# Kernel optimization log

Measured on AMD Instinct MI355X. Metric: run time of the kernel, lower is better.

Reference implementation:

```python
import jax, jax.numpy as jnp
import numpy as np

N_NODES = 50000
N_EDGES = 600000
DIM_H = 128
LN_EPS = 1e-5


def setup_inputs() -> dict:
    key = jax.random.key(0)
    ks = jax.random.split(key, 8)
    s = 1.0 / np.sqrt(DIM_H)
    return {
        "nodes": jax.random.normal(ks[0], (N_NODES, DIM_H), jnp.float32),
        "W_msg": jax.random.normal(ks[1], (DIM_H, DIM_H), jnp.float32) * s,
        "b_msg": jnp.zeros((DIM_H,), jnp.float32),
        "w_ih": jax.random.normal(ks[2], (3 * DIM_H, DIM_H), jnp.float32) * s,
        "w_hh": jax.random.normal(ks[3], (3 * DIM_H, DIM_H), jnp.float32) * s,
        "b_ih": jnp.zeros((3 * DIM_H,), jnp.float32),
        "b_hh": jnp.zeros((3 * DIM_H,), jnp.float32),
        "ln_gamma": jnp.ones((DIM_H,), jnp.float32),
        "ln_beta": jnp.zeros((DIM_H,), jnp.float32),
        "edge_src": jax.random.randint(ks[4], (N_EDGES,), 0, N_NODES, jnp.int32),
        "edge_dst": jax.random.randint(ks[5], (N_EDGES,), 0, N_NODES, jnp.int32),
    }


def _layer_norm(x, gamma, beta):
    mu = jnp.mean(x, axis=-1, keepdims=True)
    var = jnp.mean(jnp.square(x - mu), axis=-1, keepdims=True)
    return gamma * (x - mu) * jax.lax.rsqrt(var + LN_EPS) + beta


def reference(nodes, W_msg, b_msg, w_ih, w_hh, b_ih, b_hh, ln_gamma, ln_beta,
              edge_src, edge_dst):
    n_nodes = nodes.shape[0]
    # send_and_recv: per-edge message from source node, sum-reduce at dest
    msg_e = nodes[edge_src] @ W_msg.T + b_msg            # [E, H] (irregular gather)
    messages = jax.ops.segment_sum(msg_e, edge_dst, num_segments=n_nodes)  # [N, H]
    # global connection: add mean node feature
    msg = messages + jnp.mean(nodes, axis=0)
    # single-step GRU (torch gate layout: r, z, n)
    gi = msg @ w_ih.T + b_ih                             # [N, 3H]
    gh = nodes @ w_hh.T + b_hh                           # [N, 3H]
    i_r, i_z, i_n = jnp.split(gi, 3, axis=-1)
    h_r, h_z, h_n = jnp.split(gh, 3, axis=-1)
    r = jax.nn.sigmoid(i_r + h_r)
    z = jax.nn.sigmoid(i_z + h_z)
    n = jnp.tanh(i_n + r * h_n)
    h_next = (1.0 - z) * n + z * nodes
    # LayerNorm then post-GRU spatial residual with messages
    out = _layer_norm(h_next, ln_gamma, ln_beta)
    out = out + messages
    return out
```

## Files before the change

kernel.cpp:

```cpp
#include <hip/hip_runtime.h>
#include <hip/hip_bf16.h>

#define N_NODES 50000
#define N_EDGES 600000
#define DIM_H   128
#define NPAD    50048
#define NB_SCAN 196

typedef __attribute__((ext_vector_type(8))) short bf16x8;
typedef __attribute__((ext_vector_type(4))) float f32x4;
typedef __attribute__((ext_vector_type(4))) short short4v;

__device__ __forceinline__ short f2bs(float f) {
    __hip_bfloat16 h = __float2bfloat16(f);
    return *reinterpret_cast<short*>(&h);
}
__device__ __forceinline__ float bs2f(short s) {
    unsigned u = ((unsigned)(unsigned short)s) << 16;
    return __builtin_bit_cast(float, u);
}
__device__ __forceinline__ float sigm(float x) { return 1.f / (1.f + __expf(-x)); }
__device__ __forceinline__ float tanh_f(float x) {
    return 2.f / (1.f + __expf(-2.f * x)) - 1.f;
}
__device__ __forceinline__ unsigned pk2(float a, float b) {
    return ((unsigned)(unsigned short)f2bs(b) << 16) | (unsigned)(unsigned short)f2bs(a);
}
__device__ __forceinline__ float unlo(unsigned u) { return bs2f((short)(u & 0xffffu)); }
__device__ __forceinline__ float unhi(unsigned u) { return bs2f((short)(u >> 16)); }

__device__ __forceinline__ void dma16(const void* g, const void* lds_uniform) {
    __builtin_amdgcn_global_load_lds(
        (const __attribute__((address_space(1))) void*)g,
        (__attribute__((address_space(3))) void*)(unsigned)(unsigned long long)lds_uniform,
        16, 0, 0);
}

__global__ __launch_bounds__(256) void prep_k(int* __restrict__ cnt,
                                              float* __restrict__ colsum,
                                              short* __restrict__ aggTail,
                                              short* __restrict__ nodesTail) {
    int i = blockIdx.x * 256 + threadIdx.x;
    if (i < N_NODES) cnt[i] = 0;
    if (i < 128) colsum[i] = 0.f;
    if (i < 1536) {
        short4v z = {0, 0, 0, 0};
        *(short4v*)(aggTail   + i * 4) = z;
        *(short4v*)(nodesTail + i * 4) = z;
    }
}

__global__ __launch_bounds__(256) void ch_k(const float* __restrict__ nodes,
                                            float* __restrict__ colsum,
                                            short* __restrict__ nodesB,
                                            const int* __restrict__ edst,
                                            int* __restrict__ cnt) {
    const int tid = threadIdx.x;
    {
        int e = (blockIdx.x * 256 + tid) * 4;
        if (e + 3 < N_EDGES) {
            int4 d = *(const int4*)(edst + e);
            atomicAdd(&cnt[d.x], 1); atomicAdd(&cnt[d.y], 1);
            atomicAdd(&cnt[d.z], 1); atomicAdd(&cnt[d.w], 1);
        } else {
            for (; e < N_EDGES; ++e) atomicAdd(&cnt[edst[e]], 1);
        }
    }
    __shared__ float red[8][128];
    const int cg = tid & 31;
    const int rl = tid >> 5;
    float4 acc = {0.f, 0.f, 0.f, 0.f};
    for (int r = blockIdx.x * 8 + rl; r < N_NODES; r += gridDim.x * 8) {
        float4 v = *(const float4*)(nodes + (size_t)r * DIM_H + cg * 4);
        acc.x += v.x; acc.y += v.y; acc.z += v.z; acc.w += v.w;
        *(short4v*)(nodesB + (size_t)r * DIM_H + cg * 4) =
            (short4v){f2bs(v.x), f2bs(v.y), f2bs(v.z), f2bs(v.w)};
    }
    *(float4*)&red[rl][cg * 4] = acc;
    __syncthreads();
    if (tid < 128) {
        float s = 0.f;
#pragma unroll
        for (int i = 0; i < 8; ++i) s += red[i][tid];
        unsafeAtomicAdd(&colsum[tid], s);
    }
}

__global__ __launch_bounds__(256) void scan_k(const int* __restrict__ cnt,
                                              int* __restrict__ rowptr,
                                              int* __restrict__ pos,
                                              const float* __restrict__ wmsg,
                                              const float* __restrict__ wih,
                                              const float* __restrict__ whh,
                                              short* __restrict__ wmsgB,
                                              short* __restrict__ wihB,
                                              short* __restrict__ whhB) {
    const int b = blockIdx.x, t = threadIdx.x;
    const int lane = t & 63, w = t >> 6;
    __shared__ int red[4];
    __shared__ int wsum[4];

    {
        const int gid = b * 256 + t;
        const int gsz = NB_SCAN * 256;
        for (int i = gid; i < 49152; i += gsz) {
            wihB[i] = f2bs(wih[i]);
            whhB[i] = f2bs(whh[i]);
        }
        if (gid < 16384) wmsgB[gid] = f2bs(wmsg[gid]);
    }

    int tot = 0;
    const int lim = b * 256;
    for (int i = t * 4; i < lim; i += 1024) {
        int4 v = *(const int4*)(cnt + i);
        tot += (v.x + v.y) + (v.z + v.w);
    }
#pragma unroll
    for (int o = 32; o; o >>= 1) tot += __shfl_xor(tot, o, 64);
    if (lane == 0) red[w] = tot;
    __syncthreads();
    const int offset = red[0] + red[1] + red[2] + red[3];

    int i = b * 256 + t;
    int v = (i < N_NODES) ? cnt[i] : 0;
    int x = v;
#pragma unroll
    for (int o = 1; o < 64; o <<= 1) {
        int y = __shfl_up(x, o, 64);
        if (lane >= o) x += y;
    }
    if (lane == 63) wsum[w] = x;
    __syncthreads();
    int woff = 0;
#pragma unroll
    for (int j = 0; j < 4; ++j)
        if (j < w) woff += wsum[j];
    int excl = offset + woff + (x - v);
    if (i < N_NODES) { rowptr[i] = excl; pos[i] = excl; }
    if (i == N_NODES - 1) rowptr[N_NODES] = excl + v;
}

__global__ __launch_bounds__(256) void reorder_k(const int* __restrict__ esrc,
                                                 const int* __restrict__ edst,
                                                 int* __restrict__ pos,
                                                 int* __restrict__ ssrc) {
    int e = (blockIdx.x * 256 + threadIdx.x) * 4;
    if (e + 3 < N_EDGES) {
        int4 s = *(const int4*)(esrc + e);
        int4 d = *(const int4*)(edst + e);
        ssrc[atomicAdd(&pos[d.x], 1)] = s.x;
        ssrc[atomicAdd(&pos[d.y], 1)] = s.y;
        ssrc[atomicAdd(&pos[d.z], 1)] = s.z;
        ssrc[atomicAdd(&pos[d.w], 1)] = s.w;
    } else {
        for (; e < N_EDGES; ++e) {
            int p = atomicAdd(&pos[edst[e]], 1);
            ssrc[p] = esrc[e];
        }
    }
}

__global__ __launch_bounds__(256) void aggregate_k(const short* __restrict__ nodesB,
                                                   const int* __restrict__ rowptr,
                                                   const int* __restrict__ ssrc,
                                                   short* __restrict__ aggB) {
    const int wid = threadIdx.x >> 6;
    const int lane = threadIdx.x & 63;
    const int g = lane >> 4, l = lane & 15;
    const int n = blockIdx.x * 4 + wid;
    if (n >= N_NODES) return;
    const int s0 = rowptr[n], s1 = rowptr[n + 1];

    float accf[8] = {0.f, 0.f, 0.f, 0.f, 0.f, 0.f, 0.f, 0.f};
    int e = s0 + g;
    for (; e + 4 < s1; e += 8) {
        int sa = ssrc[e], sb = ssrc[e + 4];
        bf16x8 va = *(const bf16x8*)(nodesB + (size_t)sa * DIM_H + l * 8);
        bf16x8 vb = *(const bf16x8*)(nodesB + (size_t)sb * DIM_H + l * 8);
#pragma unroll
        for (int k = 0; k < 8; ++k) accf[k] += bs2f(va[k]) + bs2f(vb[k]);
    }
    if (e < s1) {
        int sa = ssrc[e];
        bf16x8 va = *(const bf16x8*)(nodesB + (size_t)sa * DIM_H + l * 8);
#pragma unroll
        for (int k = 0; k < 8; ++k) accf[k] += bs2f(va[k]);
    }
#pragma unroll
    for (int k = 0; k < 8; ++k) {
        accf[k] += __shfl_xor(accf[k], 32, 64);
        accf[k] += __shfl_xor(accf[k], 16, 64);
    }
    if (g == 0) {
        uint4 ov;
        ov.x = pk2(accf[0], accf[1]);
        ov.y = pk2(accf[2], accf[3]);
        ov.z = pk2(accf[4], accf[5]);
        ov.w = pk2(accf[6], accf[7]);
        *(uint4*)(aggB + (size_t)n * DIM_H + l * 8) = ov;
    }
}

__global__ __launch_bounds__(512) void fused_k(const short* __restrict__ aggB,
                                               const short* __restrict__ nodesB,
                                               const short* __restrict__ wmsgB,
                                               const short* __restrict__ wihB,
                                               const short* __restrict__ whhB,
                                               const float* __restrict__ bmsg,
                                               const float* __restrict__ bih,
                                               const float* __restrict__ bhh,
                                               const int* __restrict__ deg,
                                               const float* __restrict__ colsum,
                                               const float* __restrict__ gamma,
                                               const float* __restrict__ beta,
                                               float* __restrict__ out) {
    __shared__ short Ms[128 * 128];
    __shared__ short Wb[2][64 * 128];
    __shared__ float biasL[1280];

    const int tid = threadIdx.x;
    const int lane = tid & 63, w = tid >> 6;
    const int m0 = blockIdx.x * 128;
    const int r16 = lane & 15, qh = lane >> 4;
    const int wm = w * 16;
    const float invN = 1.0f / N_NODES;

    if (tid < 384) {
        biasL[tid]       = bih[tid];
        biasL[384 + tid] = bhh[tid];
    }
    if (tid < 128) {
        biasL[768  + tid] = bmsg[tid];
        biasL[896  + tid] = colsum[tid] * invN;
        biasL[1024 + tid] = gamma[tid];
        biasL[1152 + tid] = beta[tid];
    }

    bf16x8 aggF[4], nodF[4], msgF[4];
    const size_t rowA = (size_t)(m0 + wm + r16) * 128;
#pragma unroll
    for (int kt = 0; kt < 4; ++kt) {
        aggF[kt] = *(const bf16x8*)(aggB   + rowA + ((kt << 2) + qh) * 8);
        nodF[kt] = *(const bf16x8*)(nodesB + rowA + ((kt << 2) + qh) * 8);
    }
    int4 dgi = *(const int4*)(deg + m0 + wm + qh * 4);

#define STAGE_W(SRC, ROW0, BUF) do {                                         \
    _Pragma("unroll") for (int it = 0; it < 2; ++it) {                       \
        int c = w * 2 + it;                                                  \
        int s = c * 64 + lane;                                               \
        int r = s >> 4, q = s & 15;                                          \
        int g = q ^ (r & 15);                                                \
        dma16((SRC) + (((size_t)((ROW0) + r)) << 7) + (g << 3),              \
              &Wb[BUF][0] + (size_t)c * 512);                                \
    } } while (0)

    STAGE_W(wmsgB, 0, 0);

    f32x4 acc[2][4];
    unsigned rp[2][4][2], inp[2][4][2], np_[2][4][2];

#define CHUNK(BUF, AF, H, RST) do {                                          \
    __builtin_amdgcn_s_setprio(1);                                           \
    _Pragma("unroll") for (int kt = 0; kt < 4; ++kt) {                       \
        const int sq = (((kt << 2) + qh) ^ r16) << 3;                        \
        bf16x8 b0 = *(const bf16x8*)&Wb[BUF][(r16     ) * 128 + sq];         \
        bf16x8 b1 = *(const bf16x8*)&Wb[BUF][(r16 + 16) * 128 + sq];         \
        bf16x8 b2 = *(const bf16x8*)&Wb[BUF][(r16 + 32) * 128 + sq];         \
        bf16x8 b3 = *(const bf16x8*)&Wb[BUF][(r16 + 48) * 128 + sq];         \
        f32x4 z4 = {0.f, 0.f, 0.f, 0.f};                                     \
        acc[H][0] = __builtin_amdgcn_mfma_f32_16x16x32_bf16(                 \
            AF[kt], b0, ((RST) && kt == 0) ? z4 : acc[H][0], 0, 0, 0);       \
        acc[H][1] = __builtin_amdgcn_mfma_f32_16x16x32_bf16(                 \
            AF[kt], b1, ((RST) && kt == 0) ? z4 : acc[H][1], 0, 0, 0);       \
        acc[H][2] = __builtin_amdgcn_mfma_f32_16x16x32_bf16(                 \
            AF[kt], b2, ((RST) && kt == 0) ? z4 : acc[H][2], 0, 0, 0);       \
        acc[H][3] = __builtin_amdgcn_mfma_f32_16x16x32_bf16(                 \
            AF[kt], b3, ((RST) && kt == 0) ? z4 : acc[H][3], 0, 0, 0);       \
    }                                                                        \
    __builtin_amdgcn_s_setprio(0);                                           \
    } while (0)

    __syncthreads(); STAGE_W(wmsgB,  64, 1); CHUNK(0, aggF, 0, 1);
    __syncthreads(); STAGE_W(wihB,    0, 0); CHUNK(1, aggF, 1, 1);

    {
        float dgf[4];
        dgf[0] = (m0 + wm + qh * 4 + 0 < N_NODES) ? (float)dgi.x : 0.f;
        dgf[1] = (m0 + wm + qh * 4 + 1 < N_NODES) ? (float)dgi.y : 0.f;
        dgf[2] = (m0 + wm + qh * 4 + 2 < N_NODES) ? (float)dgi.z : 0.f;
        dgf[3] = (m0 + wm + qh * 4 + 3 < N_NODES) ? (float)dgi.w : 0.f;
#pragma unroll
        for (int h = 0; h < 2; ++h)
#pragma unroll
            for (int j = 0; j < 4; ++j) {
                int c = h * 64 + j * 16 + r16;
                float bm = biasL[768 + c], cs = biasL[896 + c];
#pragma unroll
                for (int rr = 0; rr < 4; ++rr) {
                    int lr = wm + qh * 4 + rr;
                    float v = acc[h][j][rr] + dgf[rr] * bm + cs;
                    int slot = (c >> 3) ^ (lr & 15);
                    Ms[lr * 128 + slot * 8 + (c & 7)] = f2bs(v);
                }
            }
#pragma unroll
        for (int kt = 0; kt < 4; ++kt) {
            int kg = (kt << 2) + qh;
            msgF[kt] = *(const bf16x8*)&Ms[(wm + r16) * 128 + ((kg ^ r16) << 3)];
        }
    }

    __syncthreads(); STAGE_W(wihB,   64, 1); CHUNK(0, msgF, 0, 1);
    __syncthreads(); STAGE_W(whhB,    0, 0); CHUNK(1, msgF, 1, 1);
    __syncthreads(); STAGE_W(whhB,   64, 1); CHUNK(0, nodF, 0, 0);
    __syncthreads(); STAGE_W(wihB,  256, 0); CHUNK(1, nodF, 1, 0);
#pragma unroll
    for (int h = 0; h < 2; ++h)
#pragma unroll
        for (int j = 0; j < 4; ++j) {
            int c = h * 64 + j * 16 + r16;
            float b0 = biasL[c] + biasL[384 + c];
            rp[h][j][0] = pk2(sigm(acc[h][j][0] + b0), sigm(acc[h][j][1] + b0));
            rp[h][j][1] = pk2(sigm(acc[h][j][2] + b0), sigm(acc[h][j][3] + b0));
        }

    __syncthreads(); STAGE_W(wihB,  320, 1); CHUNK(0, msgF, 0, 1);
    __syncthreads(); STAGE_W(whhB,  256, 0); CHUNK(1, msgF, 1, 1);
#pragma unroll
    for (int h = 0; h < 2; ++h)
#pragma unroll
        for (int j = 0; j < 4; ++j) {
            int c = h * 64 + j * 16 + r16;
            float bi = biasL[256 + c];
            inp[h][j][0] = pk2(acc[h][j][0] + bi, acc[h][j][1] + bi);
            inp[h][j][1] = pk2(acc[h][j][2] + bi, acc[h][j][3] + bi);
        }

    __syncthreads(); STAGE_W(whhB,  320, 1); CHUNK(0, nodF, 0, 1);
    __syncthreads(); STAGE_W(wihB,  128, 0); CHUNK(1, nodF, 1, 1);
#pragma unroll
    for (int h = 0; h < 2; ++h)
#pragma unroll
        for (int j = 0; j < 4; ++j) {
            int c = h * 64 + j * 16 + r16;
            float bh = biasL[640 + c];
            float n0 = tanh_f(unlo(inp[h][j][0]) + unlo(rp[h][j][0]) * (acc[h][j][0] + bh));
            float n1 = tanh_f(unhi(inp[h][j][0]) + unhi(rp[h][j][0]) * (acc[h][j][1] + bh));
            float n2 = tanh_f(unlo(inp[h][j][1]) + unlo(rp[h][j][1]) * (acc[h][j][2] + bh));
            float n3 = tanh_f(unhi(inp[h][j][1]) + unhi(rp[h][j][1]) * (acc[h][j][3] + bh));
            np_[h][j][0] = pk2(n0, n1);
            np_[h][j][1] = pk2(n2, n3);
        }

    __syncthreads(); STAGE_W(wihB,  192, 1); CHUNK(0, msgF, 0, 1);
    __syncthreads(); STAGE_W(whhB,  128, 0); CHUNK(1, msgF, 1, 1);
    __syncthreads(); STAGE_W(whhB,  192, 1); CHUNK(0, nodF, 0, 0);
    __syncthreads();                         CHUNK(1, nodF, 1, 0);

#pragma unroll
    for (int h = 0; h < 2; ++h)
#pragma unroll
        for (int j = 0; j < 4; ++j) {
            int c = h * 64 + j * 16 + r16;
            float b1 = biasL[128 + c] + biasL[512 + c];
#pragma unroll
            for (int rr = 0; rr < 4; ++rr) {
                int lr = wm + qh * 4 + rr;
                float hv = bs2f(nodesB[(size_t)(m0 + lr) * 128 + c]);
                float z = sigm(acc[h][j][rr] + b1);
                float nv = (rr & 1) ? unhi(np_[h][j][rr >> 1]) : unlo(np_[h][j][rr >> 1]);
                acc[h][j][rr] = (1.f - z) * nv + z * hv;
            }
        }

#pragma unroll
    for (int rr = 0; rr < 4; ++rr) {
        float s = 0.f, q2 = 0.f;
#pragma unroll
        for (int h = 0; h < 2; ++h)
#pragma unroll
            for (int j = 0; j < 4; ++j) {
                float v = acc[h][j][rr];
                s += v; q2 += v * v;
            }
#pragma unroll
        for (int o = 1; o < 16; o <<= 1) {
            s  += __shfl_xor(s, o, 64);
            q2 += __shfl_xor(q2, o, 64);
        }
        int lr = wm + qh * 4 + rr;
        int gm = m0 + lr;
        float mu = s * (1.0f / DIM_H);
        float var = q2 * (1.0f / DIM_H) - mu * mu;
        float rstd = rsqrtf(var + 1e-5f);
        if (gm < N_NODES) {
#pragma unroll
            for (int h = 0; h < 2; ++h)
#pragma unroll
                for (int j = 0; j < 4; ++j) {
                    int c = h * 64 + j * 16 + r16;
                    int slot = (c >> 3) ^ (lr & 15);
                    float resid = bs2f(Ms[lr * 128 + slot * 8 + (c & 7)])
                                - biasL[896 + c];
                    out[(size_t)gm * DIM_H + c] =
                        biasL[1024 + c] * (acc[h][j][rr] - mu) * rstd
                        + biasL[1152 + c] + resid;
                }
        }
    }
#undef CHUNK
#undef STAGE_W
}

extern "C" void kernel_launch(void* const* d_in, const int* in_sizes, int n_in,
                              void* d_out, int out_size, void* d_ws, size_t ws_size,
                              hipStream_t stream) {
    const float* nodes = (const float*)d_in[0];
    const float* Wmsg  = (const float*)d_in[1];
    const float* bmsg  = (const float*)d_in[2];
    const float* wih   = (const float*)d_in[3];
    const float* whh   = (const float*)d_in[4];
    const float* bih   = (const float*)d_in[5];
    const float* bhh   = (const float*)d_in[6];
    const float* gamma = (const float*)d_in[7];
    const float* beta  = (const float*)d_in[8];
    const int* esrc = (const int*)d_in[9];
    const int* edst = (const int*)d_in[10];
    float* out = (float*)d_out;

    char* ws = (char*)d_ws;
    short* aggB   = (short*)ws;
    short* nodesB = (short*)(ws + 12812288);
    short* wmsgB  = (short*)(ws + 25624576);
    short* wihB   = (short*)(ws + 25657344);
    short* whhB   = (short*)(ws + 25755648);
    float* colsum = (float*)(ws + 25853952);
    int*   cnt    = (int*)(ws + 25854464);
    int*   rowptr = (int*)(ws + 26054464);
    int*   pos    = (int*)(ws + 26254480);
    int*   ssrc   = (int*)(ws + 26454480);

    short* aggTail   = aggB   + (size_t)N_NODES * DIM_H;
    short* nodesTail = nodesB + (size_t)N_NODES * DIM_H;

    prep_k<<<NB_SCAN, 256, 0, stream>>>(cnt, colsum, aggTail, nodesTail);

    const int EB4 = (N_EDGES / 4 + 255) / 256;
    ch_k<<<EB4, 256, 0, stream>>>(nodes, colsum, nodesB, edst, cnt);
    scan_k<<<NB_SCAN, 256, 0, stream>>>(cnt, rowptr, pos,
                                        Wmsg, wih, whh, wmsgB, wihB, whhB);
    reorder_k<<<EB4, 256, 0, stream>>>(esrc, edst, pos, ssrc);
    aggregate_k<<<(N_NODES + 3) / 4, 256, 0, stream>>>(nodesB, rowptr, ssrc, aggB);

    const int MB = (N_NODES + 127) / 128;
    fused_k<<<MB, 512, 0, stream>>>(aggB, nodesB, wmsgB, wihB, whhB,
                                    bmsg, bih, bhh, cnt, colsum, gamma, beta, out);
}
```

Measured before the change: 237.3 us.

## Fuse edge aggregation into GEMM kernel via LDS, drop aggregate kernel

Removes the separate aggregate_k kernel and the bf16 aggB intermediate buffer. The fused GEMM/GRU kernel now gathers and sums neighbour rows itself for each of its 128 rows, writes the sums into the swizzled Ms LDS tile, and reads A fragments from there. The per-node gather now uses one 16-lane group walking all edges with int4 index loads and eight outstanding row loads, instead of four groups splitting the edges. It also drops the s_setprio calls around the MFMA chunks. This saves a launch and a global write/read round trip of the aggregate, at the cost of doing the irregular gather inside a 512-thread kernel with only 391 blocks, which may hide latency less well.

```diff
diff --git a/kernel.cpp b/kernel.cpp
--- a/kernel.cpp
+++ b/kernel.cpp
@@ -38,14 +38,12 @@
 
 __global__ __launch_bounds__(256) void prep_k(int* __restrict__ cnt,
                                               float* __restrict__ colsum,
-                                              short* __restrict__ aggTail,
                                               short* __restrict__ nodesTail) {
     int i = blockIdx.x * 256 + threadIdx.x;
     if (i < N_NODES) cnt[i] = 0;
     if (i < 128) colsum[i] = 0.f;
     if (i < 1536) {
         short4v z = {0, 0, 0, 0};
-        *(short4v*)(aggTail   + i * 4) = z;
         *(short4v*)(nodesTail + i * 4) = z;
     }
 }
@@ -161,49 +159,9 @@
     }
 }
 
-__global__ __launch_bounds__(256) void aggregate_k(const short* __restrict__ nodesB,
-                                                   const int* __restrict__ rowptr,
-                                                   const int* __restrict__ ssrc,
-                                                   short* __restrict__ aggB) {
-    const int wid = threadIdx.x >> 6;
-    const int lane = threadIdx.x & 63;
-    const int g = lane >> 4, l = lane & 15;
-    const int n = blockIdx.x * 4 + wid;
-    if (n >= N_NODES) return;
-    const int s0 = rowptr[n], s1 = rowptr[n + 1];
-
-    float accf[8] = {0.f, 0.f, 0.f, 0.f, 0.f, 0.f, 0.f, 0.f};
-    int e = s0 + g;
-    for (; e + 4 < s1; e += 8) {
-        int sa = ssrc[e], sb = ssrc[e + 4];
-        bf16x8 va = *(const bf16x8*)(nodesB + (size_t)sa * DIM_H + l * 8);
-        bf16x8 vb = *(const bf16x8*)(nodesB + (size_t)sb * DIM_H + l * 8);
-#pragma unroll
-        for (int k = 0; k < 8; ++k) accf[k] += bs2f(va[k]) + bs2f(vb[k]);
-    }
-    if (e < s1) {
-        int sa = ssrc[e];
-        bf16x8 va = *(const bf16x8*)(nodesB + (size_t)sa * DIM_H + l * 8);
-#pragma unroll
-        for (int k = 0; k < 8; ++k) accf[k] += bs2f(va[k]);
-    }
-#pragma unroll
-    for (int k = 0; k < 8; ++k) {
-        accf[k] += __shfl_xor(accf[k], 32, 64);
-        accf[k] += __shfl_xor(accf[k], 16, 64);
-    }
-    if (g == 0) {
-        uint4 ov;
-        ov.x = pk2(accf[0], accf[1]);
-        ov.y = pk2(accf[2], accf[3]);
-        ov.z = pk2(accf[4], accf[5]);
-        ov.w = pk2(accf[6], accf[7]);
-        *(uint4*)(aggB + (size_t)n * DIM_H + l * 8) = ov;
-    }
-}
-
-__global__ __launch_bounds__(512) void fused_k(const short* __restrict__ aggB,
-                                               const short* __restrict__ nodesB,
+__global__ __launch_bounds__(512) void fused_k(const short* __restrict__ nodesB,
+                                               const int* __restrict__ rowptr,
+                                               const int* __restrict__ ssrc,
                                                const short* __restrict__ wmsgB,
                                                const short* __restrict__ wihB,
                                                const short* __restrict__ whhB,
@@ -226,26 +184,6 @@
     const int wm = w * 16;
     const float invN = 1.0f / N_NODES;
 
-    if (tid < 384) {
-        biasL[tid]       = bih[tid];
-        biasL[384 + tid] = bhh[tid];
-    }
-    if (tid < 128) {
-        biasL[768  + tid] = bmsg[tid];
-        biasL[896  + tid] = colsum[tid] * invN;
-        biasL[1024 + tid] = gamma[tid];
-        biasL[1152 + tid] = beta[tid];
-    }
-
-    bf16x8 aggF[4], nodF[4], msgF[4];
-    const size_t rowA = (size_t)(m0 + wm + r16) * 128;
-#pragma unroll
-    for (int kt = 0; kt < 4; ++kt) {
-        aggF[kt] = *(const bf16x8*)(aggB   + rowA + ((kt << 2) + qh) * 8);
-        nodF[kt] = *(const bf16x8*)(nodesB + rowA + ((kt << 2) + qh) * 8);
-    }
-    int4 dgi = *(const int4*)(deg + m0 + wm + qh * 4);
-
 #define STAGE_W(SRC, ROW0, BUF) do {                                         \
     _Pragma("unroll") for (int it = 0; it < 2; ++it) {                       \
         int c = w * 2 + it;                                                  \
@@ -258,11 +196,70 @@
 
     STAGE_W(wmsgB, 0, 0);
 
+    if (tid < 384) {
+        biasL[tid]       = bih[tid];
+        biasL[384 + tid] = bhh[tid];
+    }
+    if (tid < 128) {
+        biasL[768  + tid] = bmsg[tid];
+        biasL[896  + tid] = colsum[tid] * invN;
+        biasL[1024 + tid] = gamma[tid];
+        biasL[1152 + tid] = beta[tid];
+    }
+
+#pragma unroll
+    for (int i = 0; i < 4; ++i) {
+        const int lr = wm + i * 4 + qh;
+        const int n = m0 + lr;
+        int s0 = 0, s1 = 0;
+        if (n < N_NODES) { s0 = rowptr[n]; s1 = rowptr[n + 1]; }
+        float accf[8] = {0.f, 0.f, 0.f, 0.f, 0.f, 0.f, 0.f, 0.f};
+        int e = s0;
+        for (; e + 7 < s1; e += 8) {
+            int4 ia = *(const int4*)(ssrc + e);
+            int4 ib = *(const int4*)(ssrc + e + 4);
+            bf16x8 va = *(const bf16x8*)(nodesB + (size_t)ia.x * DIM_H + r16 * 8);
+            bf16x8 vb = *(const bf16x8*)(nodesB + (size_t)ia.y * DIM_H + r16 * 8);
+            bf16x8 vc = *(const bf16x8*)(nodesB + (size_t)ia.z * DIM_H + r16 * 8);
+            bf16x8 vd = *(const bf16x8*)(nodesB + (size_t)ia.w * DIM_H + r16 * 8);
+            bf16x8 ve = *(const bf16x8*)(nodesB + (size_t)ib.x * DIM_H + r16 * 8);
+            bf16x8 vf = *(const bf16x8*)(nodesB + (size_t)ib.y * DIM_H + r16 * 8);
+            bf16x8 vg = *(const bf16x8*)(nodesB + (size_t)ib.z * DIM_H + r16 * 8);
+            bf16x8 vh = *(const bf16x8*)(nodesB + (size_t)ib.w * DIM_H + r16 * 8);
+#pragma unroll
+            for (int k = 0; k < 8; ++k)
+                accf[k] += ((bs2f(va[k]) + bs2f(vb[k])) + (bs2f(vc[k]) + bs2f(vd[k])))
+                         + ((bs2f(ve[k]) + bs2f(vf[k])) + (bs2f(vg[k]) + bs2f(vh[k])));
+        }
+        for (; e < s1; ++e) {
+            int sa = ssrc[e];
+            bf16x8 va = *(const bf16x8*)(nodesB + (size_t)sa * DIM_H + r16 * 8);
+#pragma unroll
+            for (int k = 0; k < 8; ++k) accf[k] += bs2f(va[k]);
+        }
+        const int slot = r16 ^ (lr & 15);
+        uint4 ov;
+        ov.x = pk2(accf[0], accf[1]);
+        ov.y = pk2(accf[2], accf[3]);
+        ov.z = pk2(accf[4], accf[5]);
+        ov.w = pk2(accf[6], accf[7]);
+        *(uint4*)&Ms[lr * 128 + slot * 8] = ov;
+    }
+
+    bf16x8 aggF[4], nodF[4], msgF[4];
+    const size_t rowA = (size_t)(m0 + wm + r16) * 128;
+#pragma unroll
+    for (int kt = 0; kt < 4; ++kt) {
+        int kg = (kt << 2) + qh;
+        aggF[kt] = *(const bf16x8*)&Ms[(wm + r16) * 128 + ((kg ^ r16) << 3)];
+        nodF[kt] = *(const bf16x8*)(nodesB + rowA + (size_t)kg * 8);
+    }
+    int4 dgi = *(const int4*)(deg + m0 + wm + qh * 4);
+
     f32x4 acc[2][4];
     unsigned rp[2][4][2], inp[2][4][2], np_[2][4][2];
 
 #define CHUNK(BUF, AF, H, RST) do {                                          \
-    __builtin_amdgcn_s_setprio(1);                                           \
     _Pragma("unroll") for (int kt = 0; kt < 4; ++kt) {                       \
         const int sq = (((kt << 2) + qh) ^ r16) << 3;                        \
         bf16x8 b0 = *(const bf16x8*)&Wb[BUF][(r16     ) * 128 + sq];         \
@@ -278,9 +275,7 @@
             AF[kt], b2, ((RST) && kt == 0) ? z4 : acc[H][2], 0, 0, 0);       \
         acc[H][3] = __builtin_amdgcn_mfma_f32_16x16x32_bf16(                 \
             AF[kt], b3, ((RST) && kt == 0) ? z4 : acc[H][3], 0, 0, 0);       \
-    }                                                                        \
-    __builtin_amdgcn_s_setprio(0);                                           \
-    } while (0)
+    } } while (0)
 
     __syncthreads(); STAGE_W(wmsgB,  64, 1); CHUNK(0, aggF, 0, 1);
     __syncthreads(); STAGE_W(wihB,    0, 0); CHUNK(1, aggF, 1, 1);
@@ -431,30 +426,27 @@
     float* out = (float*)d_out;
 
     char* ws = (char*)d_ws;
-    short* aggB   = (short*)ws;
-    short* nodesB = (short*)(ws + 12812288);
-    short* wmsgB  = (short*)(ws + 25624576);
-    short* wihB   = (short*)(ws + 25657344);
-    short* whhB   = (short*)(ws + 25755648);
-    float* colsum = (float*)(ws + 25853952);
-    int*   cnt    = (int*)(ws + 25854464);
-    int*   rowptr = (int*)(ws + 26054464);
-    int*   pos    = (int*)(ws + 26254480);
-    int*   ssrc   = (int*)(ws + 26454480);
-
-    short* aggTail   = aggB   + (size_t)N_NODES * DIM_H;
+    short* nodesB = (short*)ws;
+    short* wmsgB  = (short*)(ws + 12812288);
+    short* wihB   = (short*)(ws + 12845056);
+    short* whhB   = (short*)(ws + 12943360);
+    float* colsum = (float*)(ws + 13041664);
+    int*   cnt    = (int*)(ws + 13042176);
+    int*   rowptr = (int*)(ws + 13242176);
+    int*   pos    = (int*)(ws + 13442192);
+    int*   ssrc   = (int*)(ws + 13642192);
+
     short* nodesTail = nodesB + (size_t)N_NODES * DIM_H;
 
-    prep_k<<<NB_SCAN, 256, 0, stream>>>(cnt, colsum, aggTail, nodesTail);
+    prep_k<<<NB_SCAN, 256, 0, stream>>>(cnt, colsum, nodesTail);
 
     const int EB4 = (N_EDGES / 4 + 255) / 256;
     ch_k<<<EB4, 256, 0, stream>>>(nodes, colsum, nodesB, edst, cnt);
     scan_k<<<NB_SCAN, 256, 0, stream>>>(cnt, rowptr, pos,
                                         Wmsg, wih, whh, wmsgB, wihB, whhB);
     reorder_k<<<EB4, 256, 0, stream>>>(esrc, edst, pos, ssrc);
-    aggregate_k<<<(N_NODES + 3) / 4, 256, 0, stream>>>(nodesB, rowptr, ssrc, aggB);
 
     const int MB = (N_NODES + 127) / 128;
-    fused_k<<<MB, 512, 0, stream>>>(aggB, nodesB, wmsgB, wihB, whhB,
+    fused_k<<<MB, 512, 0, stream>>>(nodesB, rowptr, ssrc, wmsgB, wihB, whhB,
                                     bmsg, bih, bhh, cnt, colsum, gamma, beta, out);
 }
```

New measurement: 255.7 us. 1.08x slower.
